# Optimization experiments

Measured on AMD Instinct MI355X. Metric: run time of the kernel, lower is better.

## Reference

```python
import jax, jax.numpy as jnp
import numpy as np

B, S, H = 1, 2048, 5120
NH, NKV, D = 40, 8, 128
G = NH // NKV            # GQA group size (n_rep)
THETA = 500000.0         # Llama4 rope base
EPS = 1e-5               # rms_norm_eps
SCALE = D ** -0.5


def setup_inputs() -> dict:
    key = jax.random.key(0)
    k1, k2, k3 = jax.random.split(key, 3)
    hidden_states = jax.random.normal(k1, (B, S, H), jnp.float32) * 0.02
    Wqkv = jax.random.normal(k2, ((NH + 2 * NKV) * D, H), jnp.float32) * 0.02
    Wo = jax.random.normal(k3, (H, NH * D), jnp.float32) * 0.02
    w_qk = jnp.ones((D,), jnp.float32)
    positions = jnp.tile(jnp.arange(S, dtype=jnp.int32), (B, 1))
    return {"positions": positions, "hidden_states": hidden_states,
            "Wqkv": Wqkv, "Wo": Wo, "w_qk": w_qk}


def _rope_neox(x, positions):
    # x: [B, S, nheads, D]; neox style: rotate concatenated halves
    half = D // 2
    inv_freq = 1.0 / (THETA ** (jnp.arange(half, dtype=jnp.float32) * 2.0 / D))
    freqs = positions.astype(jnp.float32)[..., None] * inv_freq  # [B,S,half]
    cos = jnp.cos(freqs)[:, :, None, :]
    sin = jnp.sin(freqs)[:, :, None, :]
    x1, x2 = jnp.split(x, 2, axis=-1)
    return jnp.concatenate([x1 * cos - x2 * sin, x2 * cos + x1 * sin], axis=-1)


def _rms_norm(x, w):
    # per-head RMSNorm over head_dim (qk_norm)
    return x * jax.lax.rsqrt(jnp.mean(x * x, axis=-1, keepdims=True) + EPS) * w


def reference(positions, hidden_states, Wqkv, Wo, w_qk):
    # QKV projection (no bias)
    qkv = jnp.einsum('bsh,oh->bso', hidden_states, Wqkv)
    q, k, v = jnp.split(qkv, [NH * D, (NH + NKV) * D], axis=-1)
    q = q.reshape(B, S, NH, D)
    k = k.reshape(B, S, NKV, D)
    v = v.reshape(B, S, NKV, D)
    # iRoPE layer: apply neox RoPE, then QK-RMSNorm on roped q/k
    q = _rms_norm(_rope_neox(q, positions), w_qk)
    k = _rms_norm(_rope_neox(k, positions), w_qk)
    # causal GQA attention
    qg = q.reshape(B, S, NKV, G, D)
    scores = jnp.einsum('bqkgd,bskd->bkgqs', qg, k) * SCALE  # [B,NKV,G,S,S]
    causal = jnp.tril(jnp.ones((S, S), dtype=bool))
    scores = jnp.where(causal, scores, jnp.finfo(scores.dtype).min)
    probs = jax.nn.softmax(scores, axis=-1)
    ctx = jnp.einsum('bkgqs,bskd->bqkgd', probs, v).reshape(B, S, NH * D)
    return jnp.einsum('bso,ho->bsh', ctx, Wo)
```

## Files before the change

kernel.cpp:

```cpp
#include <hip/hip_runtime.h>

typedef unsigned short u16;
typedef __bf16 bf16x8 __attribute__((ext_vector_type(8)));
typedef float f32x4 __attribute__((ext_vector_type(4)));
typedef unsigned u32x4 __attribute__((ext_vector_type(4)));

#define S_LEN 2048
#define HID 5120
#define NHEAD 40
#define NKVH 8
#define HD 128
#define QKV_COLS 7168
#define GQA 5
#define QBLK 128
#define KVBLK 64
#define NQT (S_LEN / QBLK)
#define NITEMS (NQT * NHEAD)

__device__ __forceinline__ u16 f2bf(float f) {
  unsigned u = __float_as_uint(f);
  u += 0x7FFFu + ((u >> 16) & 1u);
  return (u16)(u >> 16);
}
__device__ __forceinline__ float bf2f(u16 v) {
  return __uint_as_float(((unsigned)v) << 16);
}

__device__ __forceinline__ void async16(void* lds, const void* g) {
  __builtin_amdgcn_global_load_lds(
      (const __attribute__((address_space(1))) unsigned int*)g,
      (__attribute__((address_space(3))) unsigned int*)lds, 16, 0, 0);
}

__global__ void k_f32_to_bf16(const float4* __restrict__ in, uint2* __restrict__ out, int n4) {
  int i = blockIdx.x * blockDim.x + threadIdx.x;
  int stride = gridDim.x * blockDim.x;
  for (; i < n4; i += stride) {
    float4 v = in[i];
    uint2 o;
    o.x = (unsigned)f2bf(v.x) | ((unsigned)f2bf(v.y) << 16);
    o.y = (unsigned)f2bf(v.z) | ((unsigned)f2bf(v.w) << 16);
    out[i] = o;
  }
}

__global__ __launch_bounds__(512, 2)
void k_gemm256(const u16* __restrict__ A, const u16* __restrict__ B,
               float* __restrict__ C, u16* __restrict__ Cb,
               int M, int N, int K) {
  __shared__ __align__(16) u16 As[2][2][128 * 64];
  __shared__ __align__(16) u16 Bs[2][2][128 * 64];
  const int tid = threadIdx.x;
  const int wave = tid >> 6, lane = tid & 63;
  const int l15 = lane & 15, l4 = lane >> 4;
  const int wm = wave >> 2, wn = wave & 3;

  const int nwg = gridDim.x;
  int f = blockIdx.x;
  int swz = (nwg % 8 == 0) ? ((f & 7) * (nwg >> 3) + (f >> 3)) : f;
  const int by = swz & 7, bx = swz >> 3;
  const int row0 = by * 256, col0 = bx * 256;

  const int srow = tid >> 3;
  const int sgch = ((tid & 7) ^ (srow & 7)) * 8;
  const int s7 = l15 & 7;
  const int ch0 = (l4 ^ s7) * 8;
  const int ch1 = ((4 + l4) ^ s7) * 8;

  f32x4 acc[8][4] = {};

#define STG_A(buf, half, kt)                                                        \
  do {                                                                              \
    const size_t k0_ = (size_t)(kt) * 64;                                           \
    async16(&As[buf][half][(wave * 8) * 64],                                        \
            A + (size_t)(row0 + (half) * 128 + srow) * K + k0_ + sgch);             \
    async16(&As[buf][half][(64 + wave * 8) * 64],                                   \
            A + (size_t)(row0 + (half) * 128 + 64 + srow) * K + k0_ + sgch);        \
  } while (0)
#define STG_B(buf, half, kt)                                                        \
  do {                                                                              \
    const size_t k0_ = (size_t)(kt) * 64;                                           \
    async16(&Bs[buf][half][(wave * 8) * 64],                                        \
            B + (size_t)(col0 + (half) * 128 + srow) * K + k0_ + sgch);             \
    async16(&Bs[buf][half][(64 + wave * 8) * 64],                                   \
            B + (size_t)(col0 + (half) * 128 + 64 + srow) * K + k0_ + sgch);        \
  } while (0)

#define PH(buf, q, STAGE, VM)                                                       \
  {                                                                                 \
    bf16x8 af[2][2];                                                                \
    _Pragma("unroll") for (int e = 0; e < 2; ++e) {                                 \
      const u16* pa = &As[buf][wm][((2 * (q) + e) * 16 + l15) * 64];                \
      af[e][0] = *(const bf16x8*)(pa + ch0);                                        \
      af[e][1] = *(const bf16x8*)(pa + ch1);                                        \
    }                                                                               \
    if ((q) == 0) {                                                                 \
      _Pragma("unroll") for (int n = 0; n < 4; ++n) {                               \
        const u16* pb = &Bs[buf][wn >> 1][((wn & 1) * 64 + n * 16 + l15) * 64];     \
        bfr[n][0] = *(const bf16x8*)(pb + ch0);                                     \
        bfr[n][1] = *(const bf16x8*)(pb + ch1);                                     \
      }                                                                             \
    }                                                                               \
    VM;                                                                             \
    __builtin_amdgcn_s_barrier();                                                   \
    asm volatile("s_waitcnt lgkmcnt(0)" ::: "memory");                              \
    STAGE;                                                                          \
    __builtin_amdgcn_s_setprio(1);                                                  \
    _Pragma("unroll") for (int kk = 0; kk < 2; ++kk)                                \
      _Pragma("unroll") for (int e = 0; e < 2; ++e)                                 \
        _Pragma("unroll") for (int n = 0; n < 4; ++n)                               \
          acc[2 * (q) + e][n] = __builtin_amdgcn_mfma_f32_16x16x32_bf16(            \
              af[e][kk], bfr[n][kk], acc[2 * (q) + e][n], 0, 0, 0);                 \
    __builtin_amdgcn_s_setprio(0);                                                  \
  }
#define VM2 asm volatile("s_waitcnt vmcnt(2)" ::: "memory")
#define VM0 asm volatile("s_waitcnt vmcnt(0)" ::: "memory")
#define VMNONE

  const int nkt = K >> 6;
  const int niter = nkt >> 1;

  STG_A(0, 0, 0); STG_A(0, 1, 0);
  STG_B(0, 0, 0); STG_B(0, 1, 0);
  STG_B(1, 0, 1); STG_B(1, 1, 1);
  asm volatile("s_waitcnt vmcnt(4)" ::: "memory");
  __builtin_amdgcn_s_barrier();

  for (int i = 0; i + 1 < niter; ++i) {
    const int t1 = 2 * i + 1, t2 = 2 * i + 2, t3 = 2 * i + 3;
    bf16x8 bfr[4][2];
    PH(0, 0, STG_A(1, 0, t1), VMNONE)
    PH(0, 1, STG_A(1, 1, t1), VMNONE)
    PH(0, 2, STG_B(0, 0, t2), VMNONE)
    PH(0, 3, STG_B(0, 1, t2), VM2)
    PH(1, 0, STG_A(0, 0, t2), VMNONE)
    PH(1, 1, STG_A(0, 1, t2), VMNONE)
    PH(1, 2, STG_B(1, 0, t3), VMNONE)
    PH(1, 3, STG_B(1, 1, t3), VM2)
  }
  {
    const int t1 = nkt - 1;
    bf16x8 bfr[4][2];
    PH(0, 0, STG_A(1, 0, t1), VMNONE)
    PH(0, 1, STG_A(1, 1, t1), VMNONE)
    PH(0, 2, ((void)0), VMNONE)
    PH(0, 3, ((void)0), VM0)
    PH(1, 0, ((void)0), VMNONE)
    PH(1, 1, ((void)0), VMNONE)
    PH(1, 2, ((void)0), VMNONE)
    PH(1, 3, ((void)0), VMNONE)
  }

  if (Cb) {
#pragma unroll
    for (int m = 0; m < 8; ++m)
#pragma unroll
      for (int n = 0; n < 4; ++n)
#pragma unroll
        for (int r = 0; r < 4; ++r) {
          int row = row0 + wm * 128 + m * 16 + l4 * 4 + r;
          int col = col0 + wn * 64 + n * 16 + l15;
          Cb[(size_t)row * N + col] = f2bf(acc[m][n][r]);
        }
  } else {
#pragma unroll
    for (int m = 0; m < 8; ++m)
#pragma unroll
      for (int n = 0; n < 4; ++n)
#pragma unroll
        for (int r = 0; r < 4; ++r) {
          int row = row0 + wm * 128 + m * 16 + l4 * 4 + r;
          int col = col0 + wn * 64 + n * 16 + l15;
          C[(size_t)row * N + col] = acc[m][n][r];
        }
  }
#undef STG_A
#undef STG_B
#undef PH
#undef VM2
#undef VM0
#undef VMNONE
}

__global__ void k_rope_norm(const u16* __restrict__ qkv, const int* __restrict__ pos,
                            const float* __restrict__ wqk,
                            u16* __restrict__ qo, u16* __restrict__ ko) {
  const int wid = (blockIdx.x * blockDim.x + threadIdx.x) >> 6;
  const int lane = threadIdx.x & 63;
  const int s = wid / 48;
  const int r = wid - s * 48;
  const u16* src;
  u16* dst;
  const bool isq = (r < NHEAD);
  if (isq) {
    src = qkv + (size_t)s * QKV_COLS + r * HD;
    dst = qo + (size_t)s * (NHEAD * HD) + r * HD;
  } else {
    int kv = r - NHEAD;
    src = qkv + (size_t)s * QKV_COLS + HID + kv * HD;
    dst = ko + (size_t)s * (NKVH * HD) + kv * HD;
  }
  float x1 = bf2f(src[lane]), x2 = bf2f(src[lane + 64]);
  float p = (float)pos[s];
  float ang = p * exp2f(-(float)lane * (18.931568569324174f / 64.0f));
  float sn, cs;
  sincosf(ang, &sn, &cs);
  float y1 = x1 * cs - x2 * sn;
  float y2 = x2 * cs + x1 * sn;
  float ss = y1 * y1 + y2 * y2;
#pragma unroll
  for (int off = 32; off > 0; off >>= 1) ss += __shfl_xor(ss, off);
  float rms = rsqrtf(ss * (1.0f / 128.0f) + 1e-5f);
  float sc = isq ? 0.08838834764831843f : 1.0f;
  dst[lane] = f2bf(y1 * rms * wqk[lane] * sc);
  dst[lane + 64] = f2bf(y2 * rms * wqk[lane + 64] * sc);
}

__global__ void k_vtrans(const u16* __restrict__ qkv, u16* __restrict__ vt) {
  __shared__ u16 t[32][132];
  const int s0 = blockIdx.x * 32;
  const int kv = blockIdx.y;
  for (int i = threadIdx.x; i < 32 * 128; i += 256) {
    int sr = i >> 7, d = i & 127;
    t[sr][d] = qkv[(size_t)(s0 + sr) * QKV_COLS + (HID + NKVH * HD) + kv * HD + d];
  }
  __syncthreads();
  for (int i = threadIdx.x; i < 32 * 128; i += 256) {
    int d = i >> 5, sc = i & 31;
    vt[((size_t)kv * HD + d) * S_LEN + s0 + sc] = t[sc][d];
  }
}

__global__ __launch_bounds__(256, 2)
void k_attn(const u16* __restrict__ Q, const u16* __restrict__ Kb,
            const u16* __restrict__ Vt, u16* __restrict__ ctx,
            int* __restrict__ counter) {
  __shared__ __align__(16) u16 Ks[2][KVBLK * HD];
  __shared__ __align__(16) u16 Vs[2][HD * KVBLK];
  __shared__ int s_item;
  const int lane = threadIdx.x & 63;
  const int wave = threadIdx.x >> 6;
  const int l15 = lane & 15, l4 = lane >> 4;
  const int l7 = lane & 7, l8 = lane >> 3;

#define STAGE_KV(KT, BUF, KVH)                                                      \
  do {                                                                             \
    const int key0_ = (KT) * KVBLK;                                                \
    _Pragma("unroll")                                                              \
    for (int i = 0; i < 4; ++i) {                                                  \
      int krow = wave * 16 + i * 4 + l4;                                           \
      int kchunk = l15 ^ (krow & 7);                                               \
      async16(&Ks[BUF][(wave * 16 + i * 4) * HD],                                  \
              Kb + (size_t)(key0_ + krow) * (NKVH * HD) + (KVH) * HD + kchunk * 8);\
    }                                                                              \
    _Pragma("unroll")                                                              \
    for (int i = 0; i < 4; ++i) {                                                  \
      int vrow = wave * 32 + i * 8 + l8;                                           \
      int vchunk = l7 ^ (vrow & 7);                                                \
      async16(&Vs[BUF][(wave * 32 + i * 8) * KVBLK],                               \
              Vt + (size_t)((KVH) * HD + vrow) * S_LEN + key0_ + vchunk * 8);      \
    }                                                                              \
  } while (0)

#define VM8 asm volatile("s_waitcnt vmcnt(8)" ::: "memory")
#define VM0 asm volatile("s_waitcnt vmcnt(0)" ::: "memory")
#define BAR __builtin_amdgcn_s_barrier(); __builtin_amdgcn_sched_barrier(0)

#define COMPUTE(BUF, KT)                                                           \
  {                                                                                \
    const int key0 = (KT) * KVBLK;                                                 \
    f32x4 sa[2][4] = {};                                                           \
    _Pragma("unroll")                                                              \
    for (int c = 0; c < 4; ++c) {                                                  \
      _Pragma("unroll")                                                            \
      for (int n = 0; n < 4; ++n) {                                                \
        const int krow = n * 16 + l15;                                             \
        bf16x8 kf = *(const bf16x8*)(&Ks[BUF][krow * HD + ((c * 4 + l4) ^ (krow & 7)) * 8]); \
        sa[0][n] = __builtin_amdgcn_mfma_f32_16x16x32_bf16(kf, qf[0][c], sa[0][n], 0, 0, 0); \
        sa[1][n] = __builtin_amdgcn_mfma_f32_16x16x32_bf16(kf, qf[1][c], sa[1][n], 0, 0, 0); \
      }                                                                            \
    }                                                                              \
    const bool domask = (key0 + KVBLK) > qt * QBLK;                                \
    bf16x8 pa[2][2];                                                               \
    _Pragma("unroll")                                                              \
    for (int m2 = 0; m2 < 2; ++m2) {                                               \
      const int qrow = qrow0 + m2 * 16 + l15;                                      \
      if (domask) {                                                                \
        _Pragma("unroll")                                                          \
        for (int n = 0; n < 4; ++n)                                                \
          _Pragma("unroll")                                                        \
          for (int r = 0; r < 4; ++r)                                              \
            if (key0 + n * 16 + l4 * 4 + r > qrow) sa[m2][n][r] = -1e30f;          \
      }                                                                            \
      float mx = sa[m2][0][0];                                                     \
      _Pragma("unroll")                                                            \
      for (int n = 0; n < 4; ++n)                                                  \
        _Pragma("unroll")                                                          \
        for (int r = 0; r < 4; ++r) mx = fmaxf(mx, sa[m2][n][r]);                  \
      mx = fmaxf(mx, __shfl_xor(mx, 16));                                          \
      mx = fmaxf(mx, __shfl_xor(mx, 32));                                          \
      const float mnew = fmaxf(m_run[m2], mx);                                     \
      const float corr = __expf(m_run[m2] - mnew);                                 \
      m_run[m2] = mnew;                                                            \
      float p[4][4];                                                               \
      float sum = 0.f;                                                             \
      _Pragma("unroll")                                                            \
      for (int n = 0; n < 4; ++n)                                                  \
        _Pragma("unroll")                                                          \
        for (int r = 0; r < 4; ++r) { p[n][r] = __expf(sa[m2][n][r] - mnew); sum += p[n][r]; } \
      sum += __shfl_xor(sum, 16);                                                  \
      sum += __shfl_xor(sum, 32);                                                  \
      l_run[m2] = l_run[m2] * corr + sum;                                          \
      _Pragma("unroll")                                                            \
      for (int r = 0; r < 4; ++r) {                                                \
        float cc = __shfl(corr, (lane & 48) + ((lane >> 4) << 2) + r);             \
        _Pragma("unroll")                                                          \
        for (int f2 = 0; f2 < 8; ++f2) oacc[m2][f2][r] *= cc;                      \
      }                                                                            \
      unsigned pkk[4][2];                                                          \
      _Pragma("unroll")                                                            \
      for (int n = 0; n < 4; ++n)                                                  \
        _Pragma("unroll")                                                          \
        for (int hi = 0; hi < 2; ++hi)                                             \
          pkk[n][hi] = (unsigned)f2bf(p[n][2 * hi]) | ((unsigned)f2bf(p[n][2 * hi + 1]) << 16); \
      const int s0l = ((lane >> 4) & 1) * 32 + (lane & 15);                        \
      const bool hiSel = (lane & 32) != 0;                                         \
      _Pragma("unroll")                                                            \
      for (int c2 = 0; c2 < 2; ++c2) {                                             \
        unsigned ox[4];                                                            \
        _Pragma("unroll")                                                          \
        for (int i = 0; i < 4; ++i) {                                              \
          int srcl = s0l + ((i >> 1) << 4);                                        \
          unsigned lo = (unsigned)__shfl((int)pkk[2 * c2][i & 1], srcl);           \
          unsigned hi2 = (unsigned)__shfl((int)pkk[2 * c2 + 1][i & 1], srcl);      \
          ox[i] = hiSel ? hi2 : lo;                                                \
        }                                                                          \
        u32x4 tmp = {ox[0], ox[1], ox[2], ox[3]};                                  \
        pa[m2][c2] = __builtin_bit_cast(bf16x8, tmp);                              \
      }                                                                            \
    }                                                                              \
    _Pragma("unroll")                                                              \
    for (int c2 = 0; c2 < 2; ++c2) {                                               \
      _Pragma("unroll")                                                            \
      for (int f2 = 0; f2 < 8; ++f2) {                                             \
        const int vrow = f2 * 16 + l15;                                            \
        bf16x8 vf = *(const bf16x8*)(&Vs[BUF][vrow * KVBLK + ((c2 * 4 + l4) ^ (vrow & 7)) * 8]); \
        oacc[0][f2] = __builtin_amdgcn_mfma_f32_16x16x32_bf16(pa[0][c2], vf, oacc[0][f2], 0, 0, 0); \
        oacc[1][f2] = __builtin_amdgcn_mfma_f32_16x16x32_bf16(pa[1][c2], vf, oacc[1][f2], 0, 0, 0); \
      }                                                                            \
    }                                                                              \
  }

  for (;;) {
    if (threadIdx.x == 0) s_item = atomicAdd(counter, 1);
    __syncthreads();
    const int item = s_item;
    if (item >= NITEMS) break;
    const int qt = (NQT - 1) - item / NHEAD;
    const int h = item % NHEAD;
    const int kvh = h / GQA;
    const int qrow0 = qt * QBLK + wave * 32;

    bf16x8 qf[2][4];
#pragma unroll
    for (int c = 0; c < 4; ++c)
#pragma unroll
      for (int m2 = 0; m2 < 2; ++m2)
        qf[m2][c] = *(const bf16x8*)(Q + (size_t)(qrow0 + m2 * 16 + l15) * HID + h * HD + c * 32 + l4 * 8);

    float m_run[2] = {-1e30f, -1e30f};
    float l_run[2] = {0.f, 0.f};
    f32x4 oacc[2][8] = {};

    const int nt = 2 * qt + 2;

    STAGE_KV(0, 0, kvh);
    STAGE_KV(1, 1, kvh);

    int t = 0;
    for (; t + 2 < nt; t += 2) {
      VM8; BAR;
      COMPUTE(0, t)
      BAR;
      STAGE_KV(t + 2, 0, kvh);
      VM8; BAR;
      COMPUTE(1, t + 1)
      BAR;
      if (t + 3 < nt) STAGE_KV(t + 3, 1, kvh);
    }
    VM8; BAR;
    COMPUTE(0, nt - 2)
    VM0; BAR;
    COMPUTE(1, nt - 1)

#pragma unroll
    for (int m2 = 0; m2 < 2; ++m2)
#pragma unroll
      for (int r = 0; r < 4; ++r) {
        float li = 1.0f / __shfl(l_run[m2], (lane & 48) + ((lane >> 4) << 2) + r);
        int row = qrow0 + m2 * 16 + l4 * 4 + r;
#pragma unroll
        for (int f2 = 0; f2 < 8; ++f2)
          ctx[(size_t)row * HID + h * HD + f2 * 16 + l15] = f2bf(oacc[m2][f2][r] * li);
      }
  }
#undef STAGE_KV
#undef VM8
#undef VM0
#undef BAR
#undef COMPUTE
}

extern "C" void kernel_launch(void* const* d_in, const int* in_sizes, int n_in,
                              void* d_out, int out_size, void* d_ws, size_t ws_size,
                              hipStream_t stream) {
  (void)in_sizes; (void)n_in; (void)out_size; (void)ws_size;
  const int* positions = (const int*)d_in[0];
  const float* hs = (const float*)d_in[1];
  const float* Wqkv = (const float*)d_in[2];
  const float* Wo = (const float*)d_in[3];
  const float* wqk = (const float*)d_in[4];
  float* out = (float*)d_out;

  char* ws = (char*)d_ws;
  u16* Wqkv_b = (u16*)ws;
  u16* q_b   = (u16*)ws;
  u16* k_b   = (u16*)(ws + 20971520);
  u16* vt_b  = (u16*)(ws + 25165824);
  int* cnt   = (int*)(ws + 29360128);
  u16* Wo_b  = (u16*)(ws + 73400320);
  u16* hs_b  = (u16*)(ws + 125829120);
  u16* ctx_b = hs_b;
  u16* qkv_b = (u16*)(ws + 146800640);

  k_f32_to_bf16<<<2048, 256, 0, stream>>>((const float4*)hs, (uint2*)hs_b, (S_LEN * HID) / 4);
  k_f32_to_bf16<<<2048, 256, 0, stream>>>((const float4*)Wqkv, (uint2*)Wqkv_b, (QKV_COLS * HID) / 4);
  k_f32_to_bf16<<<2048, 256, 0, stream>>>((const float4*)Wo, (uint2*)Wo_b, (HID * HID) / 4);

  k_gemm256<<<dim3((QKV_COLS / 256) * (S_LEN / 256)), 512, 0, stream>>>(
      hs_b, Wqkv_b, (float*)nullptr, qkv_b, S_LEN, QKV_COLS, HID);

  k_rope_norm<<<(S_LEN * 48) / 4, 256, 0, stream>>>(qkv_b, positions, wqk, q_b, k_b);
  k_vtrans<<<dim3(S_LEN / 32, NKVH), 256, 0, stream>>>(qkv_b, vt_b);

  hipMemsetAsync(cnt, 0, 4, stream);
  k_attn<<<dim3(512), 256, 0, stream>>>(q_b, k_b, vt_b, ctx_b, cnt);

  k_gemm256<<<dim3((HID / 256) * (S_LEN / 256)), 512, 0, stream>>>(
      ctx_b, Wo_b, out, (u16*)nullptr, S_LEN, HID, HID);
}
```

Baseline: 493.2 us.

## Fuse fp32-to-bf16 weight conversion into GEMM B-tile loading

```diff
diff --git a/kernel.cpp b/kernel.cpp
--- a/kernel.cpp
+++ b/kernel.cpp
@@ -45,7 +45,7 @@
 }
 
 __global__ __launch_bounds__(512, 2)
-void k_gemm256(const u16* __restrict__ A, const u16* __restrict__ B,
+void k_gemm256(const u16* __restrict__ A, const float* __restrict__ B32,
                float* __restrict__ C, u16* __restrict__ Cb,
                int M, int N, int K) {
   __shared__ __align__(16) u16 As[2][2][128 * 64];
@@ -68,6 +68,7 @@
   const int ch1 = ((4 + l4) ^ s7) * 8;
 
   f32x4 acc[8][4] = {};
+  f32x4 s0_0, s0_1, s0_2, s0_3, s1_0, s1_1, s1_2, s1_3;
 
 #define STG_A(buf, half, kt)                                                        \
   do {                                                                              \
@@ -77,13 +78,29 @@
     async16(&As[buf][half][(64 + wave * 8) * 64],                                   \
             A + (size_t)(row0 + (half) * 128 + 64 + srow) * K + k0_ + sgch);        \
   } while (0)
-#define STG_B(buf, half, kt)                                                        \
+
+#define LOADB(S, half, kt)                                                          \
   do {                                                                              \
-    const size_t k0_ = (size_t)(kt) * 64;                                           \
-    async16(&Bs[buf][half][(wave * 8) * 64],                                        \
-            B + (size_t)(col0 + (half) * 128 + srow) * K + k0_ + sgch);             \
-    async16(&Bs[buf][half][(64 + wave * 8) * 64],                                   \
-            B + (size_t)(col0 + (half) * 128 + 64 + srow) * K + k0_ + sgch);        \
+    const float* bp0_ = B32 + (size_t)(col0 + (half) * 128 + srow) * K              \
+                        + (size_t)(kt) * 64 + sgch;                                 \
+    const float* bp1_ = bp0_ + (size_t)64 * K;                                      \
+    S##_0 = *(const f32x4*)bp0_; S##_1 = *(const f32x4*)(bp0_ + 4);                 \
+    S##_2 = *(const f32x4*)bp1_; S##_3 = *(const f32x4*)(bp1_ + 4);                 \
+  } while (0)
+
+#define WRITB(S, buf, half)                                                         \
+  do {                                                                              \
+    bf16x8 w0_, w1_;                                                                \
+    w0_[0] = (__bf16)S##_0[0]; w0_[1] = (__bf16)S##_0[1];                           \
+    w0_[2] = (__bf16)S##_0[2]; w0_[3] = (__bf16)S##_0[3];                           \
+    w0_[4] = (__bf16)S##_1[0]; w0_[5] = (__bf16)S##_1[1];                           \
+    w0_[6] = (__bf16)S##_1[2]; w0_[7] = (__bf16)S##_1[3];                           \
+    w1_[0] = (__bf16)S##_2[0]; w1_[1] = (__bf16)S##_2[1];                           \
+    w1_[2] = (__bf16)S##_2[2]; w1_[3] = (__bf16)S##_2[3];                           \
+    w1_[4] = (__bf16)S##_3[0]; w1_[5] = (__bf16)S##_3[1];                           \
+    w1_[6] = (__bf16)S##_3[2]; w1_[7] = (__bf16)S##_3[3];                           \
+    *(bf16x8*)(&Bs[buf][half][srow * 64 + (tid & 7) * 8]) = w0_;                    \
+    *(bf16x8*)(&Bs[buf][half][(64 + srow) * 64 + (tid & 7) * 8]) = w1_;             \
   } while (0)
 
 #define PH(buf, q, STAGE, VM)                                                       \
@@ -113,36 +130,50 @@
               af[e][kk], bfr[n][kk], acc[2 * (q) + e][n], 0, 0, 0);                 \
     __builtin_amdgcn_s_setprio(0);                                                  \
   }
-#define VM2 asm volatile("s_waitcnt vmcnt(2)" ::: "memory")
+#define VM4 asm volatile("s_waitcnt vmcnt(4)" ::: "memory")
 #define VM0 asm volatile("s_waitcnt vmcnt(0)" ::: "memory")
 #define VMNONE
 
   const int nkt = K >> 6;
   const int niter = nkt >> 1;
 
+  LOADB(s0, 0, 0); LOADB(s1, 1, 0);
+  WRITB(s0, 0, 0); WRITB(s1, 0, 1);
+  LOADB(s0, 0, 1); LOADB(s1, 1, 1);
+  WRITB(s0, 1, 0); WRITB(s1, 1, 1);
   STG_A(0, 0, 0); STG_A(0, 1, 0);
-  STG_B(0, 0, 0); STG_B(0, 1, 0);
-  STG_B(1, 0, 1); STG_B(1, 1, 1);
-  asm volatile("s_waitcnt vmcnt(4)" ::: "memory");
+  VM0;
+  asm volatile("s_waitcnt lgkmcnt(0)" ::: "memory");
   __builtin_amdgcn_s_barrier();
 
-  for (int i = 0; i + 1 < niter; ++i) {
+  {
+    bf16x8 bfr[4][2];
+    PH(0, 0, STG_A(1, 0, 1), VMNONE)
+    PH(0, 1, STG_A(1, 1, 1), VMNONE)
+    PH(0, 2, LOADB(s0, 0, 2), VMNONE)
+    PH(0, 3, LOADB(s1, 1, 2), VM4)
+    PH(1, 0, { STG_A(0, 0, 2); WRITB(s0, 0, 0); }, VMNONE)
+    PH(1, 1, { STG_A(0, 1, 2); WRITB(s1, 0, 1); }, VMNONE)
+    PH(1, 2, LOADB(s0, 0, 3), VMNONE)
+    PH(1, 3, LOADB(s1, 1, 3), VM4)
+  }
+  for (int i = 1; i + 1 < niter; ++i) {
     const int t1 = 2 * i + 1, t2 = 2 * i + 2, t3 = 2 * i + 3;
     bf16x8 bfr[4][2];
-    PH(0, 0, STG_A(1, 0, t1), VMNONE)
-    PH(0, 1, STG_A(1, 1, t1), VMNONE)
-    PH(0, 2, STG_B(0, 0, t2), VMNONE)
-    PH(0, 3, STG_B(0, 1, t2), VM2)
-    PH(1, 0, STG_A(0, 0, t2), VMNONE)
-    PH(1, 1, STG_A(0, 1, t2), VMNONE)
-    PH(1, 2, STG_B(1, 0, t3), VMNONE)
-    PH(1, 3, STG_B(1, 1, t3), VM2)
+    PH(0, 0, { STG_A(1, 0, t1); WRITB(s0, 1, 0); }, VMNONE)
+    PH(0, 1, { STG_A(1, 1, t1); WRITB(s1, 1, 1); }, VMNONE)
+    PH(0, 2, LOADB(s0, 0, t2), VMNONE)
+    PH(0, 3, LOADB(s1, 1, t2), VM4)
+    PH(1, 0, { STG_A(0, 0, t2); WRITB(s0, 0, 0); }, VMNONE)
+    PH(1, 1, { STG_A(0, 1, t2); WRITB(s1, 0, 1); }, VMNONE)
+    PH(1, 2, LOADB(s0, 0, t3), VMNONE)
+    PH(1, 3, LOADB(s1, 1, t3), VM4)
   }
   {
     const int t1 = nkt - 1;
     bf16x8 bfr[4][2];
-    PH(0, 0, STG_A(1, 0, t1), VMNONE)
-    PH(0, 1, STG_A(1, 1, t1), VMNONE)
+    PH(0, 0, { STG_A(1, 0, t1); WRITB(s0, 1, 0); }, VMNONE)
+    PH(0, 1, { STG_A(1, 1, t1); WRITB(s1, 1, 1); }, VMNONE)
     PH(0, 2, ((void)0), VMNONE)
     PH(0, 3, ((void)0), VM0)
     PH(1, 0, ((void)0), VMNONE)
@@ -175,9 +206,10 @@
         }
   }
 #undef STG_A
-#undef STG_B
+#undef LOADB
+#undef WRITB
 #undef PH
-#undef VM2
+#undef VM4
 #undef VM0
 #undef VMNONE
 }
@@ -423,22 +455,18 @@
   float* out = (float*)d_out;
 
   char* ws = (char*)d_ws;
-  u16* Wqkv_b = (u16*)ws;
   u16* q_b   = (u16*)ws;
   u16* k_b   = (u16*)(ws + 20971520);
   u16* vt_b  = (u16*)(ws + 25165824);
   int* cnt   = (int*)(ws + 29360128);
-  u16* Wo_b  = (u16*)(ws + 73400320);
   u16* hs_b  = (u16*)(ws + 125829120);
   u16* ctx_b = hs_b;
   u16* qkv_b = (u16*)(ws + 146800640);
 
   k_f32_to_bf16<<<2048, 256, 0, stream>>>((const float4*)hs, (uint2*)hs_b, (S_LEN * HID) / 4);
-  k_f32_to_bf16<<<2048, 256, 0, stream>>>((const float4*)Wqkv, (uint2*)Wqkv_b, (QKV_COLS * HID) / 4);
-  k_f32_to_bf16<<<2048, 256, 0, stream>>>((const float4*)Wo, (uint2*)Wo_b, (HID * HID) / 4);
 
   k_gemm256<<<dim3((QKV_COLS / 256) * (S_LEN / 256)), 512, 0, stream>>>(
-      hs_b, Wqkv_b, (float*)nullptr, qkv_b, S_LEN, QKV_COLS, HID);
+      hs_b, Wqkv, (float*)nullptr, qkv_b, S_LEN, QKV_COLS, HID);
 
   k_rope_norm<<<(S_LEN * 48) / 4, 256, 0, stream>>>(qkv_b, positions, wqk, q_b, k_b);
   k_vtrans<<<dim3(S_LEN / 32, NKVH), 256, 0, stream>>>(qkv_b, vt_b);
@@ -447,5 +475,5 @@
   k_attn<<<dim3(512), 256, 0, stream>>>(q_b, k_b, vt_b, ctx_b, cnt);
 
   k_gemm256<<<dim3((HID / 256) * (S_LEN / 256)), 512, 0, stream>>>(
-      ctx_b, Wo_b, out, (u16*)nullptr, S_LEN, HID, HID);
-}
+      ctx_b, Wo, out, (u16*)nullptr, S_LEN, HID, HID);
+}
```

New measurement: 522.4 us. +5.9%, slower.

## Drop V LDS staging and persistent scheduler; read V from global, one block per item

Applied to the files above, without the earlier changes.

```diff
diff --git a/kernel.cpp b/kernel.cpp
--- a/kernel.cpp
+++ b/kernel.cpp
@@ -231,19 +231,21 @@
   }
 }
 
-__global__ __launch_bounds__(256, 2)
+__global__ __launch_bounds__(256, 4)
 void k_attn(const u16* __restrict__ Q, const u16* __restrict__ Kb,
-            const u16* __restrict__ Vt, u16* __restrict__ ctx,
-            int* __restrict__ counter) {
+            const u16* __restrict__ Vt, u16* __restrict__ ctx) {
   __shared__ __align__(16) u16 Ks[2][KVBLK * HD];
-  __shared__ __align__(16) u16 Vs[2][HD * KVBLK];
-  __shared__ int s_item;
   const int lane = threadIdx.x & 63;
   const int wave = threadIdx.x >> 6;
   const int l15 = lane & 15, l4 = lane >> 4;
-  const int l7 = lane & 7, l8 = lane >> 3;
-
-#define STAGE_KV(KT, BUF, KVH)                                                      \
+
+  const int item = blockIdx.x;
+  const int qt = (NQT - 1) - item / NHEAD;
+  const int h = item % NHEAD;
+  const int kvh = h / GQA;
+  const int qrow0 = qt * QBLK + wave * 32;
+
+#define STAGE_K(KT, BUF)                                                           \
   do {                                                                             \
     const int key0_ = (KT) * KVBLK;                                                \
     _Pragma("unroll")                                                              \
@@ -251,18 +253,11 @@
       int krow = wave * 16 + i * 4 + l4;                                           \
       int kchunk = l15 ^ (krow & 7);                                               \
       async16(&Ks[BUF][(wave * 16 + i * 4) * HD],                                  \
-              Kb + (size_t)(key0_ + krow) * (NKVH * HD) + (KVH) * HD + kchunk * 8);\
-    }                                                                              \
-    _Pragma("unroll")                                                              \
-    for (int i = 0; i < 4; ++i) {                                                  \
-      int vrow = wave * 32 + i * 8 + l8;                                           \
-      int vchunk = l7 ^ (vrow & 7);                                                \
-      async16(&Vs[BUF][(wave * 32 + i * 8) * KVBLK],                               \
-              Vt + (size_t)((KVH) * HD + vrow) * S_LEN + key0_ + vchunk * 8);      \
+              Kb + (size_t)(key0_ + krow) * (NKVH * HD) + kvh * HD + kchunk * 8);  \
     }                                                                              \
   } while (0)
 
-#define VM8 asm volatile("s_waitcnt vmcnt(8)" ::: "memory")
+#define VM4 asm volatile("s_waitcnt vmcnt(4)" ::: "memory")
 #define VM0 asm volatile("s_waitcnt vmcnt(0)" ::: "memory")
 #define BAR __builtin_amdgcn_s_barrier(); __builtin_amdgcn_sched_barrier(0)
 
@@ -339,73 +334,63 @@
         pa[m2][c2] = __builtin_bit_cast(bf16x8, tmp);                              \
       }                                                                            \
     }                                                                              \
+                           \
     _Pragma("unroll")                                                              \
     for (int c2 = 0; c2 < 2; ++c2) {                                               \
       _Pragma("unroll")                                                            \
       for (int f2 = 0; f2 < 8; ++f2) {                                             \
-        const int vrow = f2 * 16 + l15;                                            \
-        bf16x8 vf = *(const bf16x8*)(&Vs[BUF][vrow * KVBLK + ((c2 * 4 + l4) ^ (vrow & 7)) * 8]); \
+        bf16x8 vf = *(const bf16x8*)(Vt + (size_t)(kvh * HD + f2 * 16 + l15) * S_LEN \
+                                     + key0 + (c2 * 4 + l4) * 8);                  \
         oacc[0][f2] = __builtin_amdgcn_mfma_f32_16x16x32_bf16(pa[0][c2], vf, oacc[0][f2], 0, 0, 0); \
         oacc[1][f2] = __builtin_amdgcn_mfma_f32_16x16x32_bf16(pa[1][c2], vf, oacc[1][f2], 0, 0, 0); \
       }                                                                            \
     }                                                                              \
   }
 
-  for (;;) {
-    if (threadIdx.x == 0) s_item = atomicAdd(counter, 1);
-    __syncthreads();
-    const int item = s_item;
-    if (item >= NITEMS) break;
-    const int qt = (NQT - 1) - item / NHEAD;
-    const int h = item % NHEAD;
-    const int kvh = h / GQA;
-    const int qrow0 = qt * QBLK + wave * 32;
-
-    bf16x8 qf[2][4];
-#pragma unroll
-    for (int c = 0; c < 4; ++c)
-#pragma unroll
-      for (int m2 = 0; m2 < 2; ++m2)
-        qf[m2][c] = *(const bf16x8*)(Q + (size_t)(qrow0 + m2 * 16 + l15) * HID + h * HD + c * 32 + l4 * 8);
-
-    float m_run[2] = {-1e30f, -1e30f};
-    float l_run[2] = {0.f, 0.f};
-    f32x4 oacc[2][8] = {};
-
-    const int nt = 2 * qt + 2;
-
-    STAGE_KV(0, 0, kvh);
-    STAGE_KV(1, 1, kvh);
-
-    int t = 0;
-    for (; t + 2 < nt; t += 2) {
-      VM8; BAR;
-      COMPUTE(0, t)
-      BAR;
-      STAGE_KV(t + 2, 0, kvh);
-      VM8; BAR;
-      COMPUTE(1, t + 1)
-      BAR;
-      if (t + 3 < nt) STAGE_KV(t + 3, 1, kvh);
+  bf16x8 qf[2][4];
+#pragma unroll
+  for (int c = 0; c < 4; ++c)
+#pragma unroll
+    for (int m2 = 0; m2 < 2; ++m2)
+      qf[m2][c] = *(const bf16x8*)(Q + (size_t)(qrow0 + m2 * 16 + l15) * HID + h * HD + c * 32 + l4 * 8);
+
+  float m_run[2] = {-1e30f, -1e30f};
+  float l_run[2] = {0.f, 0.f};
+  f32x4 oacc[2][8] = {};
+
+  const int nt = 2 * qt + 2;
+
+  STAGE_K(0, 0);
+  STAGE_K(1, 1);
+
+  int t = 0;
+  for (; t + 2 < nt; t += 2) {
+    VM4; BAR;
+    COMPUTE(0, t)
+    BAR;
+    STAGE_K(t + 2, 0);
+    VM4; BAR;
+    COMPUTE(1, t + 1)
+    BAR;
+    if (t + 3 < nt) STAGE_K(t + 3, 1);
+  }
+  VM4; BAR;
+  COMPUTE(0, nt - 2)
+  VM0; BAR;
+  COMPUTE(1, nt - 1)
+
+#pragma unroll
+  for (int m2 = 0; m2 < 2; ++m2)
+#pragma unroll
+    for (int r = 0; r < 4; ++r) {
+      float li = 1.0f / __shfl(l_run[m2], (lane & 48) + ((lane >> 4) << 2) + r);
+      int row = qrow0 + m2 * 16 + l4 * 4 + r;
+#pragma unroll
+      for (int f2 = 0; f2 < 8; ++f2)
+        ctx[(size_t)row * HID + h * HD + f2 * 16 + l15] = f2bf(oacc[m2][f2][r] * li);
     }
-    VM8; BAR;
-    COMPUTE(0, nt - 2)
-    VM0; BAR;
-    COMPUTE(1, nt - 1)
-
-#pragma unroll
-    for (int m2 = 0; m2 < 2; ++m2)
-#pragma unroll
-      for (int r = 0; r < 4; ++r) {
-        float li = 1.0f / __shfl(l_run[m2], (lane & 48) + ((lane >> 4) << 2) + r);
-        int row = qrow0 + m2 * 16 + l4 * 4 + r;
-#pragma unroll
-        for (int f2 = 0; f2 < 8; ++f2)
-          ctx[(size_t)row * HID + h * HD + f2 * 16 + l15] = f2bf(oacc[m2][f2][r] * li);
-      }
-  }
-#undef STAGE_KV
-#undef VM8
+#undef STAGE_K
+#undef VM4
 #undef VM0
 #undef BAR
 #undef COMPUTE
@@ -427,7 +412,6 @@
   u16* q_b   = (u16*)ws;
   u16* k_b   = (u16*)(ws + 20971520);
   u16* vt_b  = (u16*)(ws + 25165824);
-  int* cnt   = (int*)(ws + 29360128);
   u16* Wo_b  = (u16*)(ws + 73400320);
   u16* hs_b  = (u16*)(ws + 125829120);
   u16* ctx_b = hs_b;
@@ -443,8 +427,7 @@
   k_rope_norm<<<(S_LEN * 48) / 4, 256, 0, stream>>>(qkv_b, positions, wqk, q_b, k_b);
   k_vtrans<<<dim3(S_LEN / 32, NKVH), 256, 0, stream>>>(qkv_b, vt_b);
 
-  hipMemsetAsync(cnt, 0, 4, stream);
-  k_attn<<<dim3(512), 256, 0, stream>>>(q_b, k_b, vt_b, ctx_b, cnt);
+  k_attn<<<dim3(NITEMS), 256, 0, stream>>>(q_b, k_b, vt_b, ctx_b);
 
   k_gemm256<<<dim3((HID / 256) * (S_LEN / 256)), 512, 0, stream>>>(
       ctx_b, Wo_b, out, (u16*)nullptr, S_LEN, HID, HID);
```

After: 829.5 us. 1.68x slower.
